# Performance work log

Hardware: AMD Instinct MI355X
Metric: run time of the kernel (lower is better)

Reference implementation:

```python
import jax, jax.numpy as jnp
import numpy as np

N, E, D, H, C = 50000, 1600000, 128, 2, 32

def setup_inputs() -> dict:
    key = jax.random.key(0)
    ks = jax.random.split(key, 8)
    x = jax.random.normal(ks[0], (N, D), jnp.float32)
    edge_index = jax.random.randint(ks[1], (2, E), 0, N)
    intra_enrichment_weights = jax.random.uniform(ks[2], (E,), jnp.float32)
    W = jax.random.normal(ks[3], (D, H * C), jnp.float32) * (1.0 / np.sqrt(D))
    att_src = jax.random.normal(ks[4], (H, C), jnp.float32) * 0.1
    att_dst = jax.random.normal(ks[5], (H, C), jnp.float32) * 0.1
    bias = jnp.zeros((H * C,), jnp.float32)
    enrichment_scale = jnp.asarray(0.01, jnp.float32)
    return dict(x=x, edge_index=edge_index,
                intra_enrichment_weights=intra_enrichment_weights,
                W=W, att_src=att_src, att_dst=att_dst, bias=bias,
                enrichment_scale=enrichment_scale)

def reference(x, edge_index, intra_enrichment_weights, W, att_src, att_dst, bias, enrichment_scale):
    n = x.shape[0]
    xf = jax.nn.elu(x)                       # F.elu on input features
    h = (xf @ W).reshape(n, H, C)            # [N, heads, out]
    # GATConv default add_self_loops=True
    loop = jnp.arange(n, dtype=edge_index.dtype)
    src = jnp.concatenate([edge_index[0], loop])
    dst = jnp.concatenate([edge_index[1], loop])
    a_src = jnp.einsum('nhc,hc->nh', h, att_src)   # [N, H]
    a_dst = jnp.einsum('nhc,hc->nh', h, att_dst)
    alpha = jax.nn.leaky_relu(a_src[src] + a_dst[dst], 0.2)  # [E+N, H]
    # softmax over incoming edges per destination node
    m = jax.ops.segment_max(alpha, dst, num_segments=n)
    e = jnp.exp(alpha - m[dst])
    denom = jax.ops.segment_sum(e, dst, num_segments=n)
    p = e / denom[dst]                       # every node has a self-loop -> denom > 0
    out = jax.ops.segment_sum(h[src] * p[:, :, None], dst, num_segments=n)  # [N, H, C]
    out = out.reshape(n, H * C) + bias
    # enrichment bias (scatter-mean of per-edge weights over source nodes)
    s0 = edge_index[0]
    nw = jax.ops.segment_sum(intra_enrichment_weights, s0, num_segments=n)
    cnt = jax.ops.segment_sum(jnp.ones_like(intra_enrichment_weights), s0, num_segments=n)
    nw = nw / jnp.maximum(cnt, 1.0)
    nw = jnp.clip(nw, 0.2, 5.0)
    scale_factor = 0.1 * jax.nn.sigmoid(enrichment_scale)
    return out + scale_factor * (nw[:, None] - 1.0)
```

## Files before the change

### kernel.cpp

```cpp
#include <hip/hip_runtime.h>


typedef unsigned int u32;
typedef unsigned short u16;

#define SLOTS3 1536
#define NB3_MAX 1600
#define EPB 4096

#define XS 136
#define CS 68

#define SMEM_F 36608

typedef __attribute__((ext_vector_type(8))) short short8;
typedef __attribute__((ext_vector_type(4))) float float4v;

__device__ __forceinline__ u16 f2bf(float f) {
    union { float f; u32 u; } v; v.f = f;
    u32 r = v.u + 0x7fffu + ((v.u >> 16) & 1u);
    return (u16)(r >> 16);
}
__device__ __forceinline__ float bf2f(u16 u) {
    union { u32 i; float f; } v; v.i = ((u32)u) << 16; return v.f;
}
__device__ __forceinline__ float bf_lo(u32 u) {
    union { u32 i; float f; } v; v.i = u << 16; return v.f;
}
__device__ __forceinline__ float bf_hi(u32 u) {
    union { u32 i; float f; } v; v.i = u & 0xFFFF0000u; return v.f;
}
__device__ __forceinline__ void bf_split(float v, short& hi, short& lo) {
    u16 h = f2bf(v);
    float hf = bf2f(h);
    hi = (short)h;
    lo = (short)f2bf(v - hf);
}

__global__ void k_prep(const float* __restrict__ Wm,
                       short* __restrict__ Whf, short* __restrict__ Wlf)
{
    int t = threadIdx.x;
    for (int p = t; p < 1024; p += 256) {
        int frag = p >> 6, l = p & 63;
        int ks = frag >> 2, nt = frag & 3;
        int q = l >> 4, m = l & 15;
        int f = nt * 16 + m;
#pragma unroll
        for (int j = 0; j < 8; ++j) {
            int k = ks * 32 + q * 8 + j;
            float wv = Wm[k * 64 + f];
            short hi, lo; bf_split(wv, hi, lo);
            Whf[p * 8 + j] = hi;
            Wlf[p * 8 + j] = lo;
        }
    }
}

static __device__ __forceinline__ void node_body(
    char* smem, int nb_id,
    const float* __restrict__ x,
    const short* __restrict__ Whf, const short* __restrict__ Wlf,
    const float* __restrict__ att_s, const float* __restrict__ att_d,
    u32* __restrict__ hb32, float* __restrict__ a_src, float* __restrict__ a_dst,
    int nN)
{
    short* Ah = (short*)smem;
    short* Al = (short*)(smem + 17408);
    float* Cl = (float*)Ah;

    int t = threadIdx.x;
    int n0 = nb_id * 64;

    for (int j = 0; j < 8; ++j) {
        int idx = t + 256 * j;
        int r = idx >> 5, c4 = idx & 31;
        int gn = n0 + r;
        float4 xv = make_float4(0.f, 0.f, 0.f, 0.f);
        if (gn < nN) xv = ((const float4*)x)[(size_t)gn * 32 + c4];
        float e[4];
        e[0] = xv.x > 0.f ? xv.x : __expf(xv.x) - 1.f;
        e[1] = xv.y > 0.f ? xv.y : __expf(xv.y) - 1.f;
        e[2] = xv.z > 0.f ? xv.z : __expf(xv.z) - 1.f;
        e[3] = xv.w > 0.f ? xv.w : __expf(xv.w) - 1.f;
        short h4[4], l4[4];
#pragma unroll
        for (int i = 0; i < 4; ++i) bf_split(e[i], h4[i], l4[i]);
        *(short4*)&Ah[r * XS + c4 * 4] = make_short4(h4[0], h4[1], h4[2], h4[3]);
        *(short4*)&Al[r * XS + c4 * 4] = make_short4(l4[0], l4[1], l4[2], l4[3]);
    }
    __syncthreads();

    {
        int w = t >> 6, l = t & 63;
        int q = l >> 4, m = l & 15;
        int arow = w * 16 + m;
        float4v acc[4] = {};
#pragma unroll
        for (int ks = 0; ks < 4; ++ks) {
            int k0 = ks * 32 + q * 8;
            short8 ah = *(const short8*)&Ah[arow * XS + k0];
            short8 al = *(const short8*)&Al[arow * XS + k0];
#pragma unroll
            for (int nt = 0; nt < 4; ++nt) {
                short8 bh = *(const short8*)&Whf[((ks * 4 + nt) * 64 + l) * 8];
                short8 bl = *(const short8*)&Wlf[((ks * 4 + nt) * 64 + l) * 8];
                acc[nt] = __builtin_amdgcn_mfma_f32_16x16x32_bf16(ah, bh, acc[nt], 0, 0, 0);
                acc[nt] = __builtin_amdgcn_mfma_f32_16x16x32_bf16(ah, bl, acc[nt], 0, 0, 0);
                acc[nt] = __builtin_amdgcn_mfma_f32_16x16x32_bf16(al, bh, acc[nt], 0, 0, 0);
            }
        }
        __syncthreads();
#pragma unroll
        for (int nt = 0; nt < 4; ++nt)
#pragma unroll
            for (int r = 0; r < 4; ++r)
                Cl[(w * 16 + q * 4 + r) * CS + nt * 16 + m] = acc[nt][r];
    }
    __syncthreads();

    {
        int nl = t >> 2, fq = t & 3;
        int gn = n0 + nl;
        float ps = 0.f, pd = 0.f;
        if (gn < nN) {
            float hv[16];
#pragma unroll
            for (int i = 0; i < 16; ++i) {
                int f = fq * 16 + i;
                hv[i] = Cl[nl * CS + f];
                ps = fmaf(hv[i], att_s[f], ps);
                pd = fmaf(hv[i], att_d[f], pd);
            }
#pragma unroll
            for (int i = 0; i < 8; ++i) {
                u32 pk = ((u32)f2bf(hv[2 * i + 1]) << 16) | (u32)f2bf(hv[2 * i]);
                hb32[(size_t)gn * 32 + fq * 8 + i] = pk;
            }
        }
        float ps2 = ps + __shfl_xor(ps, 1, 64);
        float pd2 = pd + __shfl_xor(pd, 1, 64);
        if (gn < nN && (fq & 1) == 0) {
            a_src[2 * gn + (fq >> 1)] = ps2;
            a_dst[2 * gn + (fq >> 1)] = pd2;
        }
    }
}

static __device__ __forceinline__ void partA_body(
    char* smem, int pa_id,
    const int* __restrict__ ei, const float* __restrict__ wgt,
    int* cursA, int* cursB, u32* bufA, u32* bufB, int E, int nb3)
{
    u32* arr  = (u32*)smem;
    int* cnt  = (int*)(smem + 16384);
    int* lofs = (int*)(smem + 22784);
    int* bas  = (int*)(smem + 29184);
    int* part = (int*)(smem + 35584);

    int t = threadIdx.x;
    int base = pa_id * EPB;
    int nv = min(EPB, E - base);
    int sv[16], dv[16]; float wv[16];
#pragma unroll
    for (int k = 0; k < 16; ++k) {
        int e = base + k * 256 + t;
        if (e < E) { sv[k] = ei[e]; dv[k] = ei[E + e]; wv[k] = wgt[e]; }
        else       { sv[k] = -1;    dv[k] = -1;        wv[k] = 0.f; }
    }

#pragma unroll
    for (int side = 0; side < 2; ++side) {
        int* curs = side ? cursB : cursA;
        u32* buf  = side ? bufB  : bufA;

        for (int b = t; b < nb3; b += 256) cnt[b] = 0;
        __syncthreads();
#pragma unroll
        for (int k = 0; k < 16; ++k) {
            int key = side ? sv[k] : dv[k];
            if (key >= 0) atomicAdd(&cnt[key >> 5], 1);
        }
        __syncthreads();
        for (int b = t; b < nb3; b += 256) {
            int c = cnt[b];
            if (c > 0) bas[b] = atomicAdd(&curs[b], c);
        }
        __syncthreads();
        {
            int c[8]; int s = 0;
#pragma unroll
            for (int i = 0; i < 8; ++i) {
                int bb = 8 * t + i;
                c[i] = (bb < nb3) ? cnt[bb] : 0;
                s += c[i];
            }
            part[t] = s;
            __syncthreads();
            for (int off = 1; off < 256; off <<= 1) {
                int v = (t >= off) ? part[t - off] : 0;
                __syncthreads();
                part[t] += v;
                __syncthreads();
            }
            int excl = part[t] - s;
#pragma unroll
            for (int i = 0; i < 8; ++i) {
                int bb = 8 * t + i;
                if (bb < nb3) lofs[bb] = excl;
                excl += c[i];
            }
        }
        __syncthreads();
        for (int b = t; b < nb3; b += 256) cnt[b] = 0;
        __syncthreads();
#pragma unroll
        for (int k = 0; k < 16; ++k) {
            int key = side ? sv[k] : dv[k];
            if (key >= 0) {
                int bk = key >> 5;
                int r = lofs[bk] + atomicAdd(&cnt[bk], 1);
                u32 payload;
                if (side) {
                    u32 wq = (u32)(wv[k] * 65536.f);
                    if (wq > 0xFFFFu) wq = 0xFFFFu;
                    payload = ((u32)(key & 31) << 16) | wq;
                } else {
                    payload = ((u32)(key & 31) << 16) | (u32)sv[k];
                }
                arr[r] = ((u32)bk << 21) | payload;
            }
        }
        __syncthreads();
        for (int i = t; i < nv; i += 256) {
            u32 va = arr[i];
            int bk = va >> 21;
            int g = bas[bk] + (i - lofs[bk]);
            if (g < SLOTS3) buf[(size_t)bk * SLOTS3 + g] = va & 0x1FFFFFu;
        }
        __syncthreads();
    }
}

__global__ __launch_bounds__(256) void k_fused(
    const float* __restrict__ x,
    const short* __restrict__ Whf, const short* __restrict__ Wlf,
    const float* __restrict__ att_s, const float* __restrict__ att_d,
    u32* __restrict__ hb32, float* __restrict__ a_src, float* __restrict__ a_dst,
    const int* __restrict__ ei, const float* __restrict__ wgt,
    int* cursA, int* cursB, u32* bufA, u32* bufB,
    int E, int nb3, int nblkA, int nN)
{
    __shared__ __align__(16) char smem[SMEM_F];
    int bid = blockIdx.x;
    int q3 = bid / 3;
    if ((bid % 3) == 0 && q3 < nblkA) {
        partA_body(smem, q3, ei, wgt, cursA, cursB, bufA, bufB, E, nb3);
    } else {
        int npa_before = min(q3 + ((bid % 3) ? 1 : 0), nblkA);
        node_body(smem, bid - npa_before, x, Whf, Wlf, att_s, att_d,
                  hb32, a_src, a_dst, nN);
    }
}

__global__ __launch_bounds__(256) void k_final(
    const u32* __restrict__ hb32,
    const float* __restrict__ a_src, const float* __restrict__ a_dst,
    const u32* __restrict__ bufA, const int* __restrict__ cursA,
    const u32* __restrict__ bufB, const int* __restrict__ cursB,
    const float* __restrict__ bias, const float* __restrict__ esc,
    float* __restrict__ out, int nN)
{
    __shared__ u32 st[SLOTS3];
    __shared__ u16 st2[SLOTS3];
    __shared__ int ldeg[32], lscan[32], lcur[32];
    __shared__ int usum[32], ucnt[32];

    int b = blockIdx.x, t = threadIdx.x;
    int n0 = b << 5;
    int nA = cursA[b]; if (nA > SLOTS3) nA = SLOTS3;
    int nB = cursB[b]; if (nB > SLOTS3) nB = SLOTS3;

    if (t < 32) { ldeg[t] = 0; lcur[t] = 0; usum[t] = 0; ucnt[t] = 0; }
    __syncthreads();
    for (int i = t; i < nA; i += 256) {
        u32 v = bufA[(size_t)b * SLOTS3 + i];
        st[i] = v;
        atomicAdd(&ldeg[v >> 16], 1);
    }
    for (int i = t; i < nB; i += 256) {
        u32 v = bufB[(size_t)b * SLOTS3 + i];
        atomicAdd(&usum[v >> 16], (int)(v & 0xFFFFu));
        atomicAdd(&ucnt[v >> 16], 1);
    }
    __syncthreads();
    if (t < 32) lscan[t] = ldeg[t];
    __syncthreads();
    for (int off = 1; off < 32; off <<= 1) {
        int v = 0;
        if (t < 32 && t >= off) v = lscan[t - off];
        __syncthreads();
        if (t < 32) lscan[t] += v;
        __syncthreads();
    }
    if (t < 32) lscan[t] -= ldeg[t];
    __syncthreads();
    for (int i = t; i < nA; i += 256) {
        u32 v = st[i];
        int dl = v >> 16;
        int pos = lscan[dl] + atomicAdd(&lcur[dl], 1);
        st2[pos] = (u16)(v & 0xFFFFu);
    }
    __syncthreads();

    int ws = t >> 6, lane = t & 63;
    int q = lane >> 4, fl = lane & 15, head = fl >> 3;
    const uint2* hb2 = (const uint2*)hb32;
    float escv = esc[0];
    float sf = 0.1f / (1.f + __expf(-escv));
    float4 bb = ((const float4*)bias)[fl];

    for (int dl = ws; dl < 32; dl += 4) {
        int gn = n0 + dl;
        if (gn >= nN) break;
        int beg = lscan[dl], cnt = ldeg[dl];
        float2 adv = ((const float2*)a_dst)[gn];
        float2 asv = ((const float2*)a_src)[gn];
        float t0 = asv.x + adv.x; t0 = t0 > 0.f ? t0 : 0.2f * t0;
        float t1 = asv.y + adv.y; t1 = t1 > 0.f ? t1 : 0.2f * t1;
        float es0 = __expf(t0), es1 = __expf(t1);

        float acc0 = 0.f, acc1 = 0.f, acc2 = 0.f, acc3 = 0.f;
        if (q == 0) {
            float eself = head ? es1 : es0;
            uint2 hs = hb2[(size_t)gn * 16 + fl];
            acc0 = eself * bf_lo(hs.x);
            acc1 = eself * bf_hi(hs.x);
            acc2 = eself * bf_lo(hs.y);
            acc3 = eself * bf_hi(hs.y);
        }
        float dsum = 0.f;

        for (int b0 = 0; b0 < cnt; b0 += 64) {
            int wn = cnt - b0; if (wn > 64) wn = 64;
            u32 si = (u32)gn; float e0 = 0.f, e1 = 0.f;
            if (lane < wn) {
                si = (u32)st2[beg + b0 + lane];
                float2 ap = ((const float2*)a_src)[si];
                float v0 = ap.x + adv.x; v0 = v0 > 0.f ? v0 : 0.2f * v0;
                float v1 = ap.y + adv.y; v1 = v1 > 0.f ? v1 : 0.2f * v1;
                e0 = __expf(v0); e1 = __expf(v1);
            }

            int iters = (wn + 3) >> 2;
#pragma unroll 8
            for (int k = 0; k < iters; ++k) {
                int e = 4 * k + q;
                u32 rsi = __shfl(si, e, 64);
                uint2 hv = hb2[(size_t)rsi * 16 + fl];
                float w0 = __shfl(e0, e, 64);
                float w1 = __shfl(e1, e, 64);
                float w = head ? w1 : w0;
                dsum += w;
                acc0 = fmaf(w, bf_lo(hv.x), acc0);
                acc1 = fmaf(w, bf_hi(hv.x), acc1);
                acc2 = fmaf(w, bf_lo(hv.y), acc2);
                acc3 = fmaf(w, bf_hi(hv.y), acc3);
            }
        }
        dsum += __shfl_xor(dsum, 16, 64); dsum += __shfl_xor(dsum, 32, 64);
        acc0 += __shfl_xor(acc0, 16, 64); acc0 += __shfl_xor(acc0, 32, 64);
        acc1 += __shfl_xor(acc1, 16, 64); acc1 += __shfl_xor(acc1, 32, 64);
        acc2 += __shfl_xor(acc2, 16, 64); acc2 += __shfl_xor(acc2, 32, 64);
        acc3 += __shfl_xor(acc3, 16, 64); acc3 += __shfl_xor(acc3, 32, 64);

        if (q == 0) {
            float den = (head ? es1 : es0) + dsum;
            float inv = 1.f / den;
            float cntf = (float)ucnt[dl];
            float nw = ((float)usum[dl] * (1.f / 65536.f)) / fmaxf(cntf, 1.f);
            nw = fminf(fmaxf(nw, 0.2f), 5.f);
            float en = sf * (nw - 1.f);
            float4 o;
            o.x = acc0 * inv + bb.x + en;
            o.y = acc1 * inv + bb.y + en;
            o.z = acc2 * inv + bb.z + en;
            o.w = acc3 * inv + bb.w + en;
            ((float4*)out)[(size_t)gn * 16 + fl] = o;
        }
    }
}

extern "C" void kernel_launch(void* const* d_in, const int* in_sizes, int n_in,
                              void* d_out, int out_size, void* d_ws, size_t ws_size,
                              hipStream_t stream)
{
    const float* x     = (const float*)d_in[0];
    const int*   ei    = (const int*)d_in[1];
    const float* wgt   = (const float*)d_in[2];
    const float* Wm    = (const float*)d_in[3];
    const float* att_s = (const float*)d_in[4];
    const float* att_d = (const float*)d_in[5];
    const float* bias  = (const float*)d_in[6];
    const float* esc   = (const float*)d_in[7];
    float* out = (float*)d_out;

    int nN = in_sizes[0] / 128;
    int E  = in_sizes[2];
    int NB3 = (nN + 31) / 32;

    char* p = (char*)d_ws;
    auto alloc = [&](size_t bytes) -> char* {
        char* r = p; p += (bytes + 255) & ~(size_t)255; return r;
    };
    u32*   hb32  = (u32*)  alloc((size_t)nN * 32 * 4);
    float* a_src = (float*)alloc((size_t)nN * 2 * 4);
    float* a_dst = (float*)alloc((size_t)nN * 2 * 4);
    short* Whf   = (short*)alloc(16 * 64 * 8 * 2);
    short* Wlf   = (short*)alloc(16 * 64 * 8 * 2);
    int*   cursA = (int*)  alloc(NB3_MAX * 4);
    int*   cursB = (int*)  alloc(NB3_MAX * 4);
    u32*   bufA  = (u32*)  alloc((size_t)NB3 * SLOTS3 * 4);
    u32*   bufB  = (u32*)  alloc((size_t)NB3 * SLOTS3 * 4);

    int nblkA = (E + EPB - 1) / EPB;
    int nblkN = (nN + 63) / 64;
    int nblkF = nblkA + nblkN;

    hipMemsetAsync(cursA, 0, (size_t)((char*)bufA - (char*)cursA), stream);
    k_prep<<<dim3(1), dim3(256), 0, stream>>>(Wm, Whf, Wlf);
    k_fused<<<dim3(nblkF), dim3(256), 0, stream>>>(x, Whf, Wlf, att_s, att_d,
                                                   hb32, a_src, a_dst,
                                                   ei, wgt, cursA, cursB, bufA, bufB,
                                                   E, NB3, nblkA, nN);
    k_final<<<dim3(NB3), dim3(256), 0, stream>>>(hb32, a_src, a_dst, bufA, cursA,
                                                 bufB, cursB, bias, esc, out, nN);
}
```

Before: 181.0 us.

## Coarsen edge partition buckets to 128 nodes and filter per 32-node subblock

The edge partitioning pass now buckets edges by groups of 128 destination/source nodes instead of 32, which shrinks the per-block histogram, scan and global cursor atomics. The final kernel launches four blocks per bucket, and each block scans the whole bucket and keeps only entries for its 32-node subrange. The separate memset is folded into the prep kernel. In exchange, each final block reads four times as much bucket data and filters most of it away, and bucket overflow now depends on the larger SLOTS capacity.

```diff
diff --git a/kernel.cpp b/kernel.cpp
--- a/kernel.cpp
+++ b/kernel.cpp
@@ -4,14 +4,15 @@
 typedef unsigned int u32;
 typedef unsigned short u16;
 
+#define SLOTS 4864
+#define NB_MAX 400
 #define SLOTS3 1536
-#define NB3_MAX 1600
 #define EPB 4096
 
 #define XS 136
 #define CS 68
 
-#define SMEM_F 36608
+#define SMEM_F 34816
 
 typedef __attribute__((ext_vector_type(8))) short short8;
 typedef __attribute__((ext_vector_type(4))) float float4v;
@@ -38,9 +39,11 @@
 }
 
 __global__ void k_prep(const float* __restrict__ Wm,
-                       short* __restrict__ Whf, short* __restrict__ Wlf)
+                       short* __restrict__ Whf, short* __restrict__ Wlf,
+                       int* cursA, int* cursB)
 {
     int t = threadIdx.x;
+    for (int i = t; i < NB_MAX; i += 256) { cursA[i] = 0; cursB[i] = 0; }
     for (int p = t; p < 1024; p += 256) {
         int frag = p >> 6, l = p & 63;
         int ks = frag >> 2, nt = frag & 3;
@@ -150,13 +153,13 @@
 static __device__ __forceinline__ void partA_body(
     char* smem, int pa_id,
     const int* __restrict__ ei, const float* __restrict__ wgt,
-    int* cursA, int* cursB, u32* bufA, u32* bufB, int E, int nb3)
+    int* cursA, int* cursB, u32* bufA, u32* bufB, int E, int nb)
 {
     u32* arr  = (u32*)smem;
     int* cnt  = (int*)(smem + 16384);
-    int* lofs = (int*)(smem + 22784);
-    int* bas  = (int*)(smem + 29184);
-    int* part = (int*)(smem + 35584);
+    int* lofs = (int*)(smem + 17984);
+    int* bas  = (int*)(smem + 19584);
+    int* part = (int*)(smem + 21184);
 
     int t = threadIdx.x;
     int base = pa_id * EPB;
@@ -174,28 +177,24 @@
         int* curs = side ? cursB : cursA;
         u32* buf  = side ? bufB  : bufA;
 
-        for (int b = t; b < nb3; b += 256) cnt[b] = 0;
+        for (int b = t; b < nb; b += 256) cnt[b] = 0;
         __syncthreads();
 #pragma unroll
         for (int k = 0; k < 16; ++k) {
             int key = side ? sv[k] : dv[k];
-            if (key >= 0) atomicAdd(&cnt[key >> 5], 1);
-        }
-        __syncthreads();
-        for (int b = t; b < nb3; b += 256) {
+            if (key >= 0) atomicAdd(&cnt[key >> 7], 1);
+        }
+        __syncthreads();
+        for (int b = t; b < nb; b += 256) {
             int c = cnt[b];
             if (c > 0) bas[b] = atomicAdd(&curs[b], c);
         }
         __syncthreads();
         {
-            int c[8]; int s = 0;
-#pragma unroll
-            for (int i = 0; i < 8; ++i) {
-                int bb = 8 * t + i;
-                c[i] = (bb < nb3) ? cnt[bb] : 0;
-                s += c[i];
-            }
-            part[t] = s;
+            int b0 = 2 * t, b1 = 2 * t + 1;
+            int c0 = (b0 < nb) ? cnt[b0] : 0;
+            int c1 = (b1 < nb) ? cnt[b1] : 0;
+            part[t] = c0 + c1;
             __syncthreads();
             for (int off = 1; off < 256; off <<= 1) {
                 int v = (t >= off) ? part[t - off] : 0;
@@ -203,40 +202,36 @@
                 part[t] += v;
                 __syncthreads();
             }
-            int excl = part[t] - s;
-#pragma unroll
-            for (int i = 0; i < 8; ++i) {
-                int bb = 8 * t + i;
-                if (bb < nb3) lofs[bb] = excl;
-                excl += c[i];
-            }
-        }
-        __syncthreads();
-        for (int b = t; b < nb3; b += 256) cnt[b] = 0;
+            int excl = part[t] - (c0 + c1);
+            if (b0 < nb) lofs[b0] = excl;
+            if (b1 < nb) lofs[b1] = excl + c0;
+        }
+        __syncthreads();
+        for (int b = t; b < nb; b += 256) cnt[b] = 0;
         __syncthreads();
 #pragma unroll
         for (int k = 0; k < 16; ++k) {
             int key = side ? sv[k] : dv[k];
             if (key >= 0) {
-                int bk = key >> 5;
+                int bk = key >> 7;
                 int r = lofs[bk] + atomicAdd(&cnt[bk], 1);
                 u32 payload;
                 if (side) {
                     u32 wq = (u32)(wv[k] * 65536.f);
                     if (wq > 0xFFFFu) wq = 0xFFFFu;
-                    payload = ((u32)(key & 31) << 16) | wq;
+                    payload = ((u32)(key & 127) << 16) | wq;
                 } else {
-                    payload = ((u32)(key & 31) << 16) | (u32)sv[k];
+                    payload = ((u32)(key & 127) << 16) | (u32)sv[k];
                 }
-                arr[r] = ((u32)bk << 21) | payload;
+                arr[r] = ((u32)bk << 23) | payload;
             }
         }
         __syncthreads();
         for (int i = t; i < nv; i += 256) {
             u32 va = arr[i];
-            int bk = va >> 21;
+            int bk = va >> 23;
             int g = bas[bk] + (i - lofs[bk]);
-            if (g < SLOTS3) buf[(size_t)bk * SLOTS3 + g] = va & 0x1FFFFFu;
+            if (g < SLOTS) buf[(size_t)bk * SLOTS + g] = va & 0x7FFFFFu;
         }
         __syncthreads();
     }
@@ -249,13 +244,13 @@
     u32* __restrict__ hb32, float* __restrict__ a_src, float* __restrict__ a_dst,
     const int* __restrict__ ei, const float* __restrict__ wgt,
     int* cursA, int* cursB, u32* bufA, u32* bufB,
-    int E, int nb3, int nblkA, int nN)
+    int E, int nb, int nblkA, int nN)
 {
     __shared__ __align__(16) char smem[SMEM_F];
     int bid = blockIdx.x;
     int q3 = bid / 3;
     if ((bid % 3) == 0 && q3 < nblkA) {
-        partA_body(smem, q3, ei, wgt, cursA, cursB, bufA, bufB, E, nb3);
+        partA_body(smem, q3, ei, wgt, cursA, cursB, bufA, bufB, E, nb);
     } else {
         int npa_before = min(q3 + ((bid % 3) ? 1 : 0), nblkA);
         node_body(smem, bid - npa_before, x, Whf, Wlf, att_s, att_d,
@@ -271,27 +266,30 @@
     const float* __restrict__ bias, const float* __restrict__ esc,
     float* __restrict__ out, int nN)
 {
-    __shared__ u32 st[SLOTS3];
     __shared__ u16 st2[SLOTS3];
     __shared__ int ldeg[32], lscan[32], lcur[32];
     __shared__ int usum[32], ucnt[32];
 
-    int b = blockIdx.x, t = threadIdx.x;
-    int n0 = b << 5;
-    int nA = cursA[b]; if (nA > SLOTS3) nA = SLOTS3;
-    int nB = cursB[b]; if (nB > SLOTS3) nB = SLOTS3;
+    int bc = blockIdx.x >> 2, sub = blockIdx.x & 3;
+    int t = threadIdx.x;
+    int n0 = (bc << 7) + (sub << 5);
+    int nA = cursA[bc]; if (nA > SLOTS) nA = SLOTS;
+    int nB = cursB[bc]; if (nB > SLOTS) nB = SLOTS;
+    const u32* bA = bufA + (size_t)bc * SLOTS;
+    const u32* bB = bufB + (size_t)bc * SLOTS;
 
     if (t < 32) { ldeg[t] = 0; lcur[t] = 0; usum[t] = 0; ucnt[t] = 0; }
     __syncthreads();
     for (int i = t; i < nA; i += 256) {
-        u32 v = bufA[(size_t)b * SLOTS3 + i];
-        st[i] = v;
-        atomicAdd(&ldeg[v >> 16], 1);
+        u32 v = bA[i];
+        if ((int)(v >> 21) == sub) atomicAdd(&ldeg[(v >> 16) & 31], 1);
     }
     for (int i = t; i < nB; i += 256) {
-        u32 v = bufB[(size_t)b * SLOTS3 + i];
-        atomicAdd(&usum[v >> 16], (int)(v & 0xFFFFu));
-        atomicAdd(&ucnt[v >> 16], 1);
+        u32 v = bB[i];
+        if ((int)(v >> 21) == sub) {
+            atomicAdd(&usum[(v >> 16) & 31], (int)(v & 0xFFFFu));
+            atomicAdd(&ucnt[(v >> 16) & 31], 1);
+        }
     }
     __syncthreads();
     if (t < 32) lscan[t] = ldeg[t];
@@ -306,10 +304,12 @@
     if (t < 32) lscan[t] -= ldeg[t];
     __syncthreads();
     for (int i = t; i < nA; i += 256) {
-        u32 v = st[i];
-        int dl = v >> 16;
-        int pos = lscan[dl] + atomicAdd(&lcur[dl], 1);
-        st2[pos] = (u16)(v & 0xFFFFu);
+        u32 v = bA[i];
+        if ((int)(v >> 21) == sub) {
+            int dl = (v >> 16) & 31;
+            int pos = lscan[dl] + atomicAdd(&lcur[dl], 1);
+            if (pos < SLOTS3) st2[pos] = (u16)(v & 0xFFFFu);
+        }
     }
     __syncthreads();
 
@@ -407,7 +407,7 @@
 
     int nN = in_sizes[0] / 128;
     int E  = in_sizes[2];
-    int NB3 = (nN + 31) / 32;
+    int NB = (nN + 127) / 128;
 
     char* p = (char*)d_ws;
     auto alloc = [&](size_t bytes) -> char* {
@@ -418,21 +418,20 @@
     float* a_dst = (float*)alloc((size_t)nN * 2 * 4);
     short* Whf   = (short*)alloc(16 * 64 * 8 * 2);
     short* Wlf   = (short*)alloc(16 * 64 * 8 * 2);
-    int*   cursA = (int*)  alloc(NB3_MAX * 4);
-    int*   cursB = (int*)  alloc(NB3_MAX * 4);
-    u32*   bufA  = (u32*)  alloc((size_t)NB3 * SLOTS3 * 4);
-    u32*   bufB  = (u32*)  alloc((size_t)NB3 * SLOTS3 * 4);
+    int*   cursA = (int*)  alloc(NB_MAX * 4);
+    int*   cursB = (int*)  alloc(NB_MAX * 4);
+    u32*   bufA  = (u32*)  alloc((size_t)NB * SLOTS * 4);
+    u32*   bufB  = (u32*)  alloc((size_t)NB * SLOTS * 4);
 
     int nblkA = (E + EPB - 1) / EPB;
     int nblkN = (nN + 63) / 64;
     int nblkF = nblkA + nblkN;
 
-    hipMemsetAsync(cursA, 0, (size_t)((char*)bufA - (char*)cursA), stream);
-    k_prep<<<dim3(1), dim3(256), 0, stream>>>(Wm, Whf, Wlf);
+    k_prep<<<dim3(1), dim3(256), 0, stream>>>(Wm, Whf, Wlf, cursA, cursB);
     k_fused<<<dim3(nblkF), dim3(256), 0, stream>>>(x, Whf, Wlf, att_s, att_d,
                                                    hb32, a_src, a_dst,
                                                    ei, wgt, cursA, cursB, bufA, bufB,
-                                                   E, NB3, nblkA, nN);
-    k_final<<<dim3(NB3), dim3(256), 0, stream>>>(hb32, a_src, a_dst, bufA, cursA,
-                                                 bufB, cursB, bias, esc, out, nN);
-}
+                                                   E, NB, nblkA, nN);
+    k_final<<<dim3(NB * 4), dim3(256), 0, stream>>>(hb32, a_src, a_dst, bufA, cursA,
+                                                    bufB, cursB, bias, esc, out, nN);
+}
```

Measured after the change: 190.1 us. +5.0%, slower.
